# Kernel optimization log

Hardware: AMD Instinct MI355X
Metric: run time of the kernel (lower is better)

Reference implementation:

```python
import jax, jax.numpy as jnp
import numpy as np

ANCHORS = np.array([116., 90., 156., 198., 373., 326.], np.float32).reshape(1, 1, 1, 3, 2)
IGNORE_THRESH = 0.5
OBJ_SCALE = 5.0
NOOBJ_SCALE = 1.0
XYWH_SCALE = 1.0
CLASS_SCALE = 1.0
GRID_SCALE = 1.0


def setup_inputs() -> dict:
    key = jax.random.key(0)
    k1, k2, k3 = jax.random.split(key, 3)
    B, GH, GW, NET, T, C = 16, 64, 64, 1024, 100, 80
    input_image = jnp.zeros((B, NET, NET, 3), jnp.float32)  # only shape is used
    y_pred = jax.random.normal(k1, (B, GH, GW, 3 * (5 + C)), jnp.float32)
    y_true = jax.random.uniform(k2, (B, GH, GW, 3, 5 + C), jnp.float32)
    true_boxes = jax.random.uniform(k3, (B, 1, 1, 1, T, 4), jnp.float32)
    return {"input_image": input_image, "y_pred": y_pred, "y_true": y_true, "true_boxes": true_boxes}


def reference(input_image, y_pred, y_true, true_boxes):
    B, GH, GW = y_true.shape[:3]
    net_h, net_w = input_image.shape[1], input_image.shape[2]
    dtype = y_pred.dtype
    anchors = jnp.asarray(ANCHORS, dtype)  # [1,1,1,3,2]
    y_pred = y_pred.reshape(B, GH, GW, 3, -1)
    object_mask = y_true[..., 4:5]  # [B,GH,GW,3,1]
    grid_factor = jnp.array([GW, GH], dtype).reshape(1, 1, 1, 1, 2)
    net_factor = jnp.array([net_w, net_h], dtype).reshape(1, 1, 1, 1, 2)
    cx, cy = jnp.meshgrid(jnp.arange(GW, dtype=dtype), jnp.arange(GH, dtype=dtype))
    cell_grid = jnp.stack([cx, cy], -1)[None, :, :, None, :]  # [1,GH,GW,1,2]

    # adjust predictions
    pred_box_xy = cell_grid + jax.nn.sigmoid(y_pred[..., :2])
    pred_box_wh = y_pred[..., 2:4]
    pred_box_conf = jax.nn.sigmoid(y_pred[..., 4:5])
    pred_box_class = y_pred[..., 5:]

    # adjust ground truth
    true_box_xy = y_true[..., 0:2]
    true_box_wh = y_true[..., 2:4]
    true_box_class = jnp.argmax(y_true[..., 5:], axis=-1)  # [B,GH,GW,3]

    # broadcast IoU: each predicted box vs all true boxes
    true_xy = true_boxes[..., 0:2] / grid_factor  # [B,1,1,1,T,2]
    true_wh = true_boxes[..., 2:4] / net_factor
    true_half = true_wh / 2.0
    true_mins, true_maxes = true_xy - true_half, true_xy + true_half
    pred_xy = (pred_box_xy / grid_factor)[..., None, :]  # [B,GH,GW,3,1,2]
    pred_wh = (jnp.exp(pred_box_wh) * anchors / net_factor)[..., None, :]
    pred_half = pred_wh / 2.0
    pred_mins, pred_maxes = pred_xy - pred_half, pred_xy + pred_half
    inter_wh = jnp.maximum(jnp.minimum(pred_maxes, true_maxes) - jnp.maximum(pred_mins, true_mins), 0.0)
    inter_area = inter_wh[..., 0] * inter_wh[..., 1]  # [B,GH,GW,3,T]
    true_area = true_wh[..., 0] * true_wh[..., 1]
    pred_area = pred_wh[..., 0] * pred_wh[..., 1]
    iou = inter_area / (pred_area + true_area - inter_area)
    best_ious = jnp.max(iou, axis=4)
    conf_ignore_mask = (best_ious > IGNORE_THRESH).astype(dtype)[..., None]

    # post-warmup branch (batch_seen > warmup_batches)
    xywh_mask = object_mask

    wh_scale = jnp.exp(true_box_wh) * anchors / net_factor
    wh_scale = (2.0 - wh_scale[..., 0] * wh_scale[..., 1])[..., None]

    xy_delta = xywh_mask * (true_box_xy - pred_box_xy) * wh_scale * XYWH_SCALE
    wh_delta = xywh_mask * (true_box_wh - pred_box_wh) * wh_scale * XYWH_SCALE
    conf_delta = (0.0 - pred_box_conf) * NOOBJ_SCALE
    conf_delta = conf_delta + object_mask * (1.0 - pred_box_conf) * OBJ_SCALE
    conf_delta = conf_delta * (1.0 - (1.0 - object_mask) * conf_ignore_mask)
    log_p = jax.nn.log_softmax(pred_box_class, axis=-1)
    ce = -jnp.take_along_axis(log_p, true_box_class[..., None], axis=-1)  # [B,GH,GW,3,1]
    class_delta = object_mask * ce * CLASS_SCALE

    delta = jnp.concatenate([xy_delta, wh_delta, conf_delta, class_delta], axis=-1)  # [B,GH,GW,3,6]
    loss = jnp.sum(jnp.square(delta), axis=(1, 2, 3, 4))
    return loss * GRID_SCALE
```

## Files before the change

kernel.cpp:

```cpp
#include <hip/hip_runtime.h>


#define NT 100
#define CPB 12288
#define NTOT 196608
#define ROWS_PER_BLOCK 64

typedef float f4 __attribute__((ext_vector_type(4)));
typedef f4 f4a __attribute__((aligned(4)));

__device__ __forceinline__ float frcp(float x) { return __builtin_amdgcn_rcpf(x); }
__device__ __forceinline__ float fsig(float x) { return frcp(1.f + __expf(-x)); }

__global__ __launch_bounds__(256) void yolo_loss_kernel(
    const float* __restrict__ y_pred,
    const float* __restrict__ y_true,
    const float* __restrict__ true_boxes,
    float* __restrict__ out)
{
    __shared__ f4 sbox[NT];
    __shared__ float swsum[4];

    const int tid = threadIdx.x;
    const int q   = tid & 3;
    const int row = blockIdx.x * ROWS_PER_BLOCK + (tid >> 2);
    const int b   = row / CPB;

    if (tid < NT) {
        const f4 tb = *(const f4*)(true_boxes + (size_t)b * NT * 4 + tid * 4);
        const float tx = tb.x * (1.f / 64.f),   ty = tb.y * (1.f / 64.f);
        const float tw = tb.z * (1.f / 1024.f), th = tb.w * (1.f / 1024.f);
        f4 r;
        r.x = tx - 0.5f * tw; r.y = ty - 0.5f * th;
        r.z = tx + 0.5f * tw; r.w = ty + 0.5f * th;
        sbox[tid] = r;
    }
    __syncthreads();

    const int rem = row % CPB;
    const int gy  = rem / 192;
    const int rr  = rem - gy * 192;
    const int gx  = rr / 3;
    const int a   = rr - gx * 3;
    const float aw = (a == 0) ? 116.f : ((a == 1) ? 156.f : 373.f);
    const float ah = (a == 0) ? 90.f  : ((a == 1) ? 198.f : 326.f);

    const float* p = y_pred + (size_t)row * 85;
    const float* t = y_true + (size_t)row * 85;

    const f4 g0 = *(const f4a*)p;
    const f4 g1 = *(const f4a*)(p + 4);
    const f4 h0 = *(const f4a*)t;
    const f4 h1 = *(const f4a*)(t + 4);

    const int ng = (q == 3) ? 4 : 5;
    f4 pg[5], tg[5];
#pragma unroll
    for (int k = 0; k < 5; ++k) {
        const int j  = 2 + q + 4 * k;
        const int jj = (j <= 20) ? j : 5;
        pg[k] = *(const f4a*)(p + 4 * jj);
        tg[k] = *(const f4a*)(t + 4 * jj);
    }
    float ptail = 0.f, ttail = 0.f;
    if (q == 3) { ptail = p[84]; ttail = t[84]; }

    const float p4v = g1.x, om = h1.x;

    float ssum = 0.f, tmax = -1e30f, psel = 0.f;
    int jm = 1 << 20;
    if (q == 0) {
#pragma unroll
        for (int e = 1; e < 4; ++e) {
            const float pv = g1[e], tv = h1[e];
            ssum += __expf(pv);
            const bool g = tv > tmax;
            tmax = g ? tv : tmax; psel = g ? pv : psel; jm = g ? (e - 1) : jm;
        }
    }
#pragma unroll
    for (int k = 0; k < 5; ++k) {
        if (k < ng) {
            const int j = 2 + q + 4 * k;
#pragma unroll
            for (int e = 0; e < 4; ++e) {
                const float pv = pg[k][e], tv = tg[k][e];
                ssum += __expf(pv);
                const bool g = tv > tmax;
                tmax = g ? tv : tmax; psel = g ? pv : psel;
                jm = g ? (4 * j + e - 5) : jm;
            }
        }
    }
    if (q == 3) {
        ssum += __expf(ptail);
        const bool g = ttail > tmax;
        tmax = g ? ttail : tmax; psel = g ? ptail : psel; jm = g ? 79 : jm;
    }
#pragma unroll
    for (int off = 1; off < 4; off <<= 1) {
        ssum += __shfl_xor(ssum, off, 64);
        const float otm = __shfl_xor(tmax, off, 64);
        const float ops = __shfl_xor(psel, off, 64);
        const int   ojm = __shfl_xor(jm, off, 64);
        const bool adopt = (otm > tmax) || (otm == tmax && ojm < jm);
        tmax = adopt ? otm : tmax; psel = adopt ? ops : psel; jm = adopt ? ojm : jm;
    }
    const float ce = __logf(ssum) - psel;

    const float predx = (float)gx + fsig(g0.x);
    const float predy = (float)gy + fsig(g0.y);
    const float conf  = fsig(p4v);
    const float pw  = __expf(g0.z) * aw * (1.f / 1024.f);
    const float phh = __expf(g0.w) * ah * (1.f / 1024.f);
    const float parea = pw * phh;
    const float px = predx * (1.f / 64.f), py = predy * (1.f / 64.f);
    const float pminx = px - 0.5f * pw,  pmaxx = px + 0.5f * pw;
    const float pminy = py - 0.5f * phh, pmaxy = py + 0.5f * phh;

    float best = 0.f;
#pragma unroll 5
    for (int k = 0; k < 25; ++k) {
        const f4 bx = sbox[q + 4 * k];
        float iw = fminf(pmaxx, bx.z) - fmaxf(pminx, bx.x);
        float ih = fminf(pmaxy, bx.w) - fmaxf(pminy, bx.y);
        iw = fmaxf(iw, 0.f); ih = fmaxf(ih, 0.f);
        const float inter = iw * ih;
        const float tarea = (bx.z - bx.x) * (bx.w - bx.y);
        best = fmaxf(best, inter * frcp(parea + tarea - inter));
    }
#pragma unroll
    for (int off = 1; off < 4; off <<= 1)
        best = fmaxf(best, __shfl_xor(best, off, 64));
    const float ignore = (best > 0.5f) ? 1.f : 0.f;

    const float wsx = __expf(h0.z) * aw * (1.f / 1024.f);
    const float wsy = __expf(h0.w) * ah * (1.f / 1024.f);
    const float ws  = 2.f - wsx * wsy;
    const float omws = om * ws;
    const float dx = omws * (h0.x - predx);
    const float dy = omws * (h0.y - predy);
    const float dw = omws * (h0.z - g0.z);
    const float dh = omws * (h0.w - g0.w);
    float dc = -conf + om * (1.f - conf) * 5.f;
    dc *= (1.f - (1.f - om) * ignore);
    const float dcl = om * ce;

    float val = dx * dx + dy * dy + dw * dw + dh * dh + dc * dc + dcl * dcl;
    val = (q == 0) ? val : 0.f;

#pragma unroll
    for (int off = 32; off > 0; off >>= 1) val += __shfl_down(val, off, 64);
    if ((tid & 63) == 0) swsum[tid >> 6] = val;
    __syncthreads();
    if (tid == 0) atomicAdd(out + b, swsum[0] + swsum[1] + swsum[2] + swsum[3]);
}

extern "C" void kernel_launch(void* const* d_in, const int* in_sizes, int n_in,
                              void* d_out, int out_size, void* d_ws, size_t ws_size,
                              hipStream_t stream) {
    const float* y_pred     = (const float*)d_in[1];
    const float* y_true     = (const float*)d_in[2];
    const float* true_boxes = (const float*)d_in[3];
    float* out = (float*)d_out;

    hipMemsetAsync(d_out, 0, (size_t)out_size * sizeof(float), stream);
    yolo_loss_kernel<<<NTOT / ROWS_PER_BLOCK, 256, 0, stream>>>(y_pred, y_true, true_boxes, out);
}
```

Measured before the change: 315.9 us.

## Stage y_pred and y_true row slabs into LDS via direct global-to-LDS loads

Each block now copies its contiguous 64-row slabs of y_pred and y_true into shared memory with 16-byte global_load_lds transfers, padding each 85-float row to 88 floats. Threads then read their vectors from LDS instead of doing strided, unaligned per-thread global loads. The goal is fully coalesced, wide global traffic that bypasses registers. The cost is about 45 KB of LDS per block, which can lower occupancy. Correctness also depends on the barrier draining the asynchronous loads before LDS is read.

```diff
diff --git a/kernel.cpp b/kernel.cpp
--- a/kernel.cpp
+++ b/kernel.cpp
@@ -5,9 +5,13 @@
 #define CPB 12288
 #define NTOT 196608
 #define ROWS_PER_BLOCK 64
+#define RPAD 88
+#define NCHUNK (ROWS_PER_BLOCK * 22)
 
 typedef float f4 __attribute__((ext_vector_type(4)));
-typedef f4 f4a __attribute__((aligned(4)));
+
+typedef const __attribute__((address_space(1))) float* gp_t;
+typedef __attribute__((address_space(3))) float* lp_t;
 
 __device__ __forceinline__ float frcp(float x) { return __builtin_amdgcn_rcpf(x); }
 __device__ __forceinline__ float fsig(float x) { return frcp(1.f + __expf(-x)); }
@@ -18,6 +22,7 @@
     const float* __restrict__ true_boxes,
     float* __restrict__ out)
 {
+    __shared__ __align__(16) float smem[2 * ROWS_PER_BLOCK * RPAD];
     __shared__ f4 sbox[NT];
     __shared__ float swsum[4];
 
@@ -25,6 +30,23 @@
     const int q   = tid & 3;
     const int row = blockIdx.x * ROWS_PER_BLOCK + (tid >> 2);
     const int b   = row / CPB;
+
+    {
+        const size_t slab = (size_t)blockIdx.x * ROWS_PER_BLOCK * 85;
+        const float* pbase = y_pred + slab;
+        const float* tbase = y_true + slab;
+#pragma unroll
+        for (int it = 0; it < 11; ++it) {
+            const int i  = tid + 256 * it;
+            const int cc = (i < NCHUNK) ? i : i - NCHUNK;
+            const float* gb = (i < NCHUNK) ? pbase : tbase;
+            const int r = cc / 22;
+            const int s = cc - 22 * r;
+            const int src = r * 85 + ((s < 21) ? 4 * s : 81);
+            __builtin_amdgcn_global_load_lds((gp_t)(gb + src),
+                                             (lp_t)(smem + 4 * i), 16, 0, 0);
+        }
+    }
 
     if (tid < NT) {
         const f4 tb = *(const f4*)(true_boxes + (size_t)b * NT * 4 + tid * 4);
@@ -45,25 +67,15 @@
     const float aw = (a == 0) ? 116.f : ((a == 1) ? 156.f : 373.f);
     const float ah = (a == 0) ? 90.f  : ((a == 1) ? 198.f : 326.f);
 
-    const float* p = y_pred + (size_t)row * 85;
-    const float* t = y_true + (size_t)row * 85;
+    const float* lp = smem + (tid >> 2) * RPAD;
+    const float* lt = smem + ROWS_PER_BLOCK * RPAD + (tid >> 2) * RPAD;
 
-    const f4 g0 = *(const f4a*)p;
-    const f4 g1 = *(const f4a*)(p + 4);
-    const f4 h0 = *(const f4a*)t;
-    const f4 h1 = *(const f4a*)(t + 4);
-
-    const int ng = (q == 3) ? 4 : 5;
-    f4 pg[5], tg[5];
-#pragma unroll
-    for (int k = 0; k < 5; ++k) {
-        const int j  = 2 + q + 4 * k;
-        const int jj = (j <= 20) ? j : 5;
-        pg[k] = *(const f4a*)(p + 4 * jj);
-        tg[k] = *(const f4a*)(t + 4 * jj);
-    }
+    const f4 g0 = *(const f4*)(lp);
+    const f4 g1 = *(const f4*)(lp + 4);
+    const f4 h0 = *(const f4*)(lt);
+    const f4 h1 = *(const f4*)(lt + 4);
     float ptail = 0.f, ttail = 0.f;
-    if (q == 3) { ptail = p[84]; ttail = t[84]; }
+    if (q == 3) { ptail = lp[87]; ttail = lt[87]; }
 
     const float p4v = g1.x, om = h1.x;
 
@@ -78,13 +90,16 @@
             tmax = g ? tv : tmax; psel = g ? pv : psel; jm = g ? (e - 1) : jm;
         }
     }
+    const int ng = (q == 3) ? 4 : 5;
 #pragma unroll
     for (int k = 0; k < 5; ++k) {
         if (k < ng) {
             const int j = 2 + q + 4 * k;
+            const f4 pv4 = *(const f4*)(lp + 4 * j);
+            const f4 tv4 = *(const f4*)(lt + 4 * j);
 #pragma unroll
             for (int e = 0; e < 4; ++e) {
-                const float pv = pg[k][e], tv = tg[k][e];
+                const float pv = pv4[e], tv = tv4[e];
                 ssum += __expf(pv);
                 const bool g = tv > tmax;
                 tmax = g ? tv : tmax; psel = g ? pv : psel;
```

After: 318.0 us. About the same (+0.7%).

## Use eight lanes per anchor row and two-stage reduction instead of atomics

Applied to the files above, without the earlier changes.

Each anchor row is now handled by 8 lanes instead of 4, so every lane loads and reduces fewer class groups and checks fewer true boxes in the IoU loop. Class vectors are loaded inside the loop instead of being preloaded into arrays, which lowers register pressure. Per-block partial sums go to a workspace, and a second small kernel reduces them per batch. This replaces the memset and the global atomics, at the cost of an extra kernel launch and twice as many blocks.

```diff
diff --git a/kernel.cpp b/kernel.cpp
--- a/kernel.cpp
+++ b/kernel.cpp
@@ -4,7 +4,9 @@
 #define NT 100
 #define CPB 12288
 #define NTOT 196608
-#define ROWS_PER_BLOCK 64
+#define ROWS_PER_BLOCK 32
+#define NBLOCKS (NTOT / ROWS_PER_BLOCK)
+#define BLOCKS_PER_B (NBLOCKS / 16)
 
 typedef float f4 __attribute__((ext_vector_type(4)));
 typedef f4 f4a __attribute__((aligned(4)));
@@ -16,14 +18,14 @@
     const float* __restrict__ y_pred,
     const float* __restrict__ y_true,
     const float* __restrict__ true_boxes,
-    float* __restrict__ out)
+    float* __restrict__ ws)
 {
     __shared__ f4 sbox[NT];
     __shared__ float swsum[4];
 
     const int tid = threadIdx.x;
-    const int q   = tid & 3;
-    const int row = blockIdx.x * ROWS_PER_BLOCK + (tid >> 2);
+    const int o   = tid & 7;
+    const int row = blockIdx.x * ROWS_PER_BLOCK + (tid >> 3);
     const int b   = row / CPB;
 
     if (tid < NT) {
@@ -53,23 +55,11 @@
     const f4 h0 = *(const f4a*)t;
     const f4 h1 = *(const f4a*)(t + 4);
 
-    const int ng = (q == 3) ? 4 : 5;
-    f4 pg[5], tg[5];
-#pragma unroll
-    for (int k = 0; k < 5; ++k) {
-        const int j  = 2 + q + 4 * k;
-        const int jj = (j <= 20) ? j : 5;
-        pg[k] = *(const f4a*)(p + 4 * jj);
-        tg[k] = *(const f4a*)(t + 4 * jj);
-    }
-    float ptail = 0.f, ttail = 0.f;
-    if (q == 3) { ptail = p[84]; ttail = t[84]; }
-
     const float p4v = g1.x, om = h1.x;
 
     float ssum = 0.f, tmax = -1e30f, psel = 0.f;
     int jm = 1 << 20;
-    if (q == 0) {
+    if (o == 7) {
 #pragma unroll
         for (int e = 1; e < 4; ++e) {
             const float pv = g1[e], tv = h1[e];
@@ -79,12 +69,14 @@
         }
     }
 #pragma unroll
-    for (int k = 0; k < 5; ++k) {
-        if (k < ng) {
-            const int j = 2 + q + 4 * k;
+    for (int k = 0; k < 3; ++k) {
+        const int j = 2 + o + 8 * k;
+        if (j <= 20) {
+            const f4 pv4 = *(const f4a*)(p + 4 * j);
+            const f4 tv4 = *(const f4a*)(t + 4 * j);
 #pragma unroll
             for (int e = 0; e < 4; ++e) {
-                const float pv = pg[k][e], tv = tg[k][e];
+                const float pv = pv4[e], tv = tv4[e];
                 ssum += __expf(pv);
                 const bool g = tv > tmax;
                 tmax = g ? tv : tmax; psel = g ? pv : psel;
@@ -92,13 +84,14 @@
             }
         }
     }
-    if (q == 3) {
-        ssum += __expf(ptail);
-        const bool g = ttail > tmax;
-        tmax = g ? ttail : tmax; psel = g ? ptail : psel; jm = g ? 79 : jm;
+    if (o == 3) {
+        const float pv = p[84], tv = t[84];
+        ssum += __expf(pv);
+        const bool g = tv > tmax;
+        tmax = g ? tv : tmax; psel = g ? pv : psel; jm = g ? 79 : jm;
     }
 #pragma unroll
-    for (int off = 1; off < 4; off <<= 1) {
+    for (int off = 1; off < 8; off <<= 1) {
         ssum += __shfl_xor(ssum, off, 64);
         const float otm = __shfl_xor(tmax, off, 64);
         const float ops = __shfl_xor(psel, off, 64);
@@ -119,25 +112,28 @@
     const float pminy = py - 0.5f * phh, pmaxy = py + 0.5f * phh;
 
     float best = 0.f;
-#pragma unroll 5
-    for (int k = 0; k < 25; ++k) {
-        const f4 bx = sbox[q + 4 * k];
-        float iw = fminf(pmaxx, bx.z) - fmaxf(pminx, bx.x);
-        float ih = fminf(pmaxy, bx.w) - fmaxf(pminy, bx.y);
-        iw = fmaxf(iw, 0.f); ih = fmaxf(ih, 0.f);
-        const float inter = iw * ih;
-        const float tarea = (bx.z - bx.x) * (bx.w - bx.y);
-        best = fmaxf(best, inter * frcp(parea + tarea - inter));
+#pragma unroll
+    for (int m = 0; m < 13; ++m) {
+        const int kk = o + 8 * m;
+        if (kk < NT) {
+            const f4 bx = sbox[kk];
+            float iw = fminf(pmaxx, bx.z) - fmaxf(pminx, bx.x);
+            float ih = fminf(pmaxy, bx.w) - fmaxf(pminy, bx.y);
+            iw = fmaxf(iw, 0.f); ih = fmaxf(ih, 0.f);
+            const float inter = iw * ih;
+            const float tarea = (bx.z - bx.x) * (bx.w - bx.y);
+            best = fmaxf(best, inter * frcp(parea + tarea - inter));
+        }
     }
 #pragma unroll
-    for (int off = 1; off < 4; off <<= 1)
+    for (int off = 1; off < 8; off <<= 1)
         best = fmaxf(best, __shfl_xor(best, off, 64));
     const float ignore = (best > 0.5f) ? 1.f : 0.f;
 
     const float wsx = __expf(h0.z) * aw * (1.f / 1024.f);
     const float wsy = __expf(h0.w) * ah * (1.f / 1024.f);
-    const float ws  = 2.f - wsx * wsy;
-    const float omws = om * ws;
+    const float wsc = 2.f - wsx * wsy;
+    const float omws = om * wsc;
     const float dx = omws * (h0.x - predx);
     const float dy = omws * (h0.y - predy);
     const float dw = omws * (h0.z - g0.z);
@@ -147,13 +143,26 @@
     const float dcl = om * ce;
 
     float val = dx * dx + dy * dy + dw * dw + dh * dh + dc * dc + dcl * dcl;
-    val = (q == 0) ? val : 0.f;
+    val = (o == 0) ? val : 0.f;
 
 #pragma unroll
     for (int off = 32; off > 0; off >>= 1) val += __shfl_down(val, off, 64);
     if ((tid & 63) == 0) swsum[tid >> 6] = val;
     __syncthreads();
-    if (tid == 0) atomicAdd(out + b, swsum[0] + swsum[1] + swsum[2] + swsum[3]);
+    if (tid == 0) ws[blockIdx.x] = swsum[0] + swsum[1] + swsum[2] + swsum[3];
+}
+
+__global__ __launch_bounds__(64) void yolo_reduce_kernel(
+    const float* __restrict__ ws, float* __restrict__ out)
+{
+    const int l = threadIdx.x;
+    const float* p = ws + blockIdx.x * BLOCKS_PER_B;
+    float v = 0.f;
+#pragma unroll
+    for (int i = 0; i < BLOCKS_PER_B / 64; ++i) v += p[l + 64 * i];
+#pragma unroll
+    for (int off = 32; off > 0; off >>= 1) v += __shfl_down(v, off, 64);
+    if (l == 0) out[blockIdx.x] = v;
 }
 
 extern "C" void kernel_launch(void* const* d_in, const int* in_sizes, int n_in,
@@ -162,8 +171,9 @@
     const float* y_pred     = (const float*)d_in[1];
     const float* y_true     = (const float*)d_in[2];
     const float* true_boxes = (const float*)d_in[3];
+    float* ws  = (float*)d_ws;
     float* out = (float*)d_out;
 
-    hipMemsetAsync(d_out, 0, (size_t)out_size * sizeof(float), stream);
-    yolo_loss_kernel<<<NTOT / ROWS_PER_BLOCK, 256, 0, stream>>>(y_pred, y_true, true_boxes, out);
+    yolo_loss_kernel<<<NBLOCKS, 256, 0, stream>>>(y_pred, y_true, true_boxes, ws);
+    yolo_reduce_kernel<<<16, 64, 0, stream>>>(ws, out);
 }
```

Result: no change. 312.8 us (-1.0%).
